# Kernel optimization log

Measured on AMD Instinct MI355X. Metric: run time of the kernel, lower is better.

Reference implementation:

```python
import jax, jax.numpy as jnp
import numpy as np

D_MODEL = 1024
D_FFN = 2048
WINDOW = 64
EPS = 1e-6


def rmsnorm(x, w):
    rms = jnp.sqrt(jnp.mean(x * x, axis=-1, keepdims=True) + EPS)
    return x / rms * w


def setup_inputs() -> dict:
    key = jax.random.key(0)
    ks = jax.random.split(key, 9)
    s = 0.02
    return {
        "x": jax.random.normal(ks[0], (4, 2048, D_MODEL), dtype=jnp.float32),
        "norm1_w": jnp.ones((D_MODEL,), dtype=jnp.float32),
        "norm2_w": jnp.ones((D_MODEL,), dtype=jnp.float32),
        "Wq": jax.random.normal(ks[1], (D_MODEL, D_MODEL), dtype=jnp.float32) * s,
        "Wk": jax.random.normal(ks[2], (D_MODEL, D_MODEL), dtype=jnp.float32) * s,
        "Wv": jax.random.normal(ks[3], (D_MODEL, D_MODEL), dtype=jnp.float32) * s,
        "Wo": jax.random.normal(ks[4], (D_MODEL, D_MODEL), dtype=jnp.float32) * s,
        "W1": jax.random.normal(ks[5], (D_MODEL, D_FFN), dtype=jnp.float32) * s,
        "W2": jax.random.normal(ks[6], (D_FFN, D_MODEL), dtype=jnp.float32) * s,
        "W3": jax.random.normal(ks[7], (D_MODEL, D_FFN), dtype=jnp.float32) * s,
    }


def reference(x, norm1_w, norm2_w, Wq, Wk, Wv, Wo, W1, W2, W3):
    B, T, D = x.shape
    scale = D ** (-0.5)
    residual = x
    xn = rmsnorm(x, norm1_w)
    q = xn @ Wq  # [B,T,D]
    k = xn @ Wk
    v = xn @ Wv
    # causal local-window mask: attend iff 0 <= i-j < WINDOW
    rows = jnp.arange(T)[:, None]
    cols = jnp.arange(T)[None, :]
    mask = (cols <= rows) & (rows - cols < WINDOW)  # [T,T] bool
    scores = jnp.einsum("bid,bjd->bij", q, k) * scale
    scores = jnp.where(mask[None], scores, -jnp.inf)
    weights = jax.nn.softmax(scores, axis=-1)
    attended = jnp.einsum("bij,bjd->bid", weights, v)
    x = residual + attended @ Wo
    # SwiGLU FFN
    xn2 = rmsnorm(x, norm2_w)
    ffn = (jax.nn.silu(xn2 @ W1) * (xn2 @ W3)) @ W2
    return x + ffn
```

## Files before the change

### kernel.cpp

```cpp
#include <hip/hip_runtime.h>
#include <hip/hip_bf16.h>

typedef __attribute__((ext_vector_type(8))) short bf16x8;
typedef __attribute__((ext_vector_type(4))) float f32x4;

__device__ __forceinline__ short to_bf16s(float f) {
    union { __hip_bfloat16 h; short s; } u;
    u.h = __float2bfloat16(f);
    return u.s;
}

__device__ __forceinline__ float bf16s_to_f(short s) {
    union { float f; unsigned u; } cv;
    cv.u = ((unsigned)(unsigned short)s) << 16;
    return cv.f;
}

__device__ __forceinline__ void load_lds16(const void* g, void* l) {
    __builtin_amdgcn_global_load_lds((const __attribute__((address_space(1))) void*)g,
                                     (__attribute__((address_space(3))) void*)l, 16, 0, 0);
}

__global__ __launch_bounds__(256)
void transpose_all(const float* __restrict__ Wq, const float* __restrict__ Wk,
                   const float* __restrict__ Wv, const float* __restrict__ Wo,
                   const float* __restrict__ W1, const float* __restrict__ W3,
                   const float* __restrict__ W2,
                   short* __restrict__ WqT, short* __restrict__ WkT,
                   short* __restrict__ WvT, short* __restrict__ WoT,
                   short* __restrict__ W1T, short* __restrict__ W3T,
                   short* __restrict__ W2T) {
    __shared__ float tile[32][33];
    const int bid = blockIdx.x;
    const float* src; short* dst; int K, N, tl;
    if (bid < 4096) {
        const int wi = bid >> 10; tl = bid & 1023;
        src = wi == 0 ? Wq : wi == 1 ? Wk : wi == 2 ? Wv : Wo;
        dst = wi == 0 ? WqT : wi == 1 ? WkT : wi == 2 ? WvT : WoT;
        K = 1024; N = 1024;
    } else if (bid < 8192) {
        const int wi = (bid - 4096) >> 11; tl = (bid - 4096) & 2047;
        src = wi ? W3 : W1; dst = wi ? W3T : W1T;
        K = 1024; N = 2048;
    } else {
        tl = bid - 8192; src = W2; dst = W2T;
        K = 2048; N = 1024;
    }
    const int nx = N >> 5;
    const int n0 = (tl % nx) * 32, k0 = (tl / nx) * 32;
    const int t = threadIdx.x;
    {
        const int lr = t >> 3, lc = (t & 7) * 4;
        float4 v = *(const float4*)&src[(long)(k0 + lr) * N + n0 + lc];
        tile[lr][lc] = v.x; tile[lr][lc + 1] = v.y;
        tile[lr][lc + 2] = v.z; tile[lr][lc + 3] = v.w;
    }
    __syncthreads();
    {
        const int nr = t >> 3, kc = (t & 7) * 4;
        short4 o;
        o.x = to_bf16s(tile[kc][nr]);
        o.y = to_bf16s(tile[kc + 1][nr]);
        o.z = to_bf16s(tile[kc + 2][nr]);
        o.w = to_bf16s(tile[kc + 3][nr]);
        *(short4*)&dst[(long)(n0 + nr) * K + k0 + kc] = o;
    }
}

__global__ __launch_bounds__(256)
void rmsnorm_kernel(const float* __restrict__ x, const float* __restrict__ wt,
                    short* __restrict__ out) {
    const int D = 1024;
    const long row = blockIdx.x;
    const int t = threadIdx.x;
    float4 v = ((const float4*)(x + row * D))[t];
    float ss = v.x * v.x + v.y * v.y + v.z * v.z + v.w * v.w;
    #pragma unroll
    for (int off = 32; off; off >>= 1) ss += __shfl_xor(ss, off);
    __shared__ float red[4];
    if ((t & 63) == 0) red[t >> 6] = ss;
    __syncthreads();
    ss = red[0] + red[1] + red[2] + red[3];
    const float inv = rsqrtf(ss * (1.0f / 1024.0f) + 1e-6f);
    float4 wv = ((const float4*)wt)[t];
    short4 o;
    o.x = to_bf16s(v.x * inv * wv.x);
    o.y = to_bf16s(v.y * inv * wv.y);
    o.z = to_bf16s(v.z * inv * wv.z);
    o.w = to_bf16s(v.w * inv * wv.w);
    *(short4*)&out[row * D + t * 4] = o;
}

#define MFMA16(MB, NB, BREG)                                                   \
    __builtin_amdgcn_s_barrier();                                              \
    asm volatile("s_waitcnt lgkmcnt(0)" ::: "memory");                         \
    __builtin_amdgcn_sched_barrier(0);                                         \
    __builtin_amdgcn_s_setprio(1);                                             \
    _Pragma("unroll")                                                          \
    for (int m_ = 0; m_ < 4; ++m_)                                             \
        _Pragma("unroll")                                                      \
        for (int n_ = 0; n_ < 2; ++n_) {                                       \
            acc[(MB) + m_][(NB) + n_] = __builtin_amdgcn_mfma_f32_16x16x32_bf16( \
                a[m_][0], BREG[n_][0], acc[(MB) + m_][(NB) + n_], 0, 0, 0);    \
            acc[(MB) + m_][(NB) + n_] = __builtin_amdgcn_mfma_f32_16x16x32_bf16( \
                a[m_][1], BREG[n_][1], acc[(MB) + m_][(NB) + n_], 0, 0, 0);    \
        }                                                                      \
    __builtin_amdgcn_s_setprio(0);                                             \
    __builtin_amdgcn_s_barrier();

#define READA(BUF, MG)                                                         \
    _Pragma("unroll")                                                          \
    for (int m_ = 0; m_ < 4; ++m_) {                                           \
        const int rih_ = ((MG) * 4 + m_) * 16 + lm;                            \
        const int rb_ = ((BUF) * 2 + wr) * 16384 + rih_ * 128;                 \
        a[m_][0] = *(const bf16x8*)&lds[rb_ + ((lk * 16) ^ sw)];               \
        a[m_][1] = *(const bf16x8*)&lds[rb_ + ((64 + lk * 16) ^ sw)];          \
    }

#define READB(BUF, NH, ARR)                                                    \
    _Pragma("unroll")                                                          \
    for (int n_ = 0; n_ < 2; ++n_) {                                           \
        const int rih_ = (wc & 1) * 64 + ((NH) * 2 + n_) * 16 + lm;            \
        const int rb_ = 65536 + ((BUF) * 2 + (wc >> 1)) * 16384 + rih_ * 128;  \
        ARR[n_][0] = *(const bf16x8*)&lds[rb_ + ((lk * 16) ^ sw)];             \
        ARR[n_][1] = *(const bf16x8*)&lds[rb_ + ((64 + lk * 16) ^ sw)];        \
    }

template<int EPI>
__global__ __launch_bounds__(512, 2)
void gemm256(const short* __restrict__ A, const short* __restrict__ B0,
             const short* __restrict__ aux, const float* __restrict__ res,
             void* __restrict__ outp, short* __restrict__ outp2,
             int M, int N, int K) {
    __shared__ __align__(16) char lds[131072];

    const int t = threadIdx.x;
    const int lane = t & 63, w = t >> 6;
    const int wr = w >> 2, wc = w & 3;
    const int lm = lane & 15, lk = lane >> 4;
    const int sw = (lm & 7) << 4;

    const int nbn = N >> 8;
    const int nwg = gridDim.x;
    const int chunk = nwg >> 3;
    const int logical = (blockIdx.x & 7) * chunk + (blockIdx.x >> 3);
    const int bm = logical / nbn, bn = logical - (logical / nbn) * nbn;

    const long Kb = (long)K * 2;
    const char* Ab = (const char*)A;
    const char* Bb = (const char*)B0;

    long srcA[2][2], srcB[2][2];
    {
        const int rowp = t >> 3;
        const int cbx = (t & 7) * 16;
        const int swz = ((t >> 3) & 7) << 4;
        #pragma unroll
        for (int h = 0; h < 2; ++h)
            #pragma unroll
            for (int c = 0; c < 2; ++c) {
                srcA[h][c] = (long)(bm * 256 + h * 128 + c * 64 + rowp) * Kb + (cbx ^ swz);
                srcB[h][c] = (long)(bn * 256 + h * 128 + c * 64 + rowp) * Kb + (cbx ^ swz);
            }
    }
    auto stA = [&](int kt, int h) {
        const int buf = kt & 1;
        #pragma unroll
        for (int c = 0; c < 2; ++c)
            load_lds16(Ab + srcA[h][c] + (long)kt * 128,
                       &lds[(buf * 2 + h) * 16384 + c * 8192 + t * 16]);
    };
    auto stB = [&](int kt, int h) {
        const int buf = kt & 1;
        #pragma unroll
        for (int c = 0; c < 2; ++c)
            load_lds16(Bb + srcB[h][c] + (long)kt * 128,
                       &lds[65536 + (buf * 2 + h) * 16384 + c * 8192 + t * 16]);
    };

    f32x4 acc[8][4] = {};
    bf16x8 a[4][2], b0[2][2], b1[2][2];
    const int nt = K >> 6;

    stB(0, 0); stB(0, 1); stA(0, 0); stA(0, 1); stB(1, 0); stB(1, 1);
    asm volatile("s_waitcnt vmcnt(4)" ::: "memory");
    __builtin_amdgcn_s_barrier();

    for (int kt0 = 0; kt0 < nt; kt0 += 2) {
        const int kt1 = kt0 + 1;
        const bool pf = (kt0 + 2) < nt;

        READA(0, 0); READB(0, 0, b0);
        stA(kt1, 0);
        MFMA16(0, 0, b0)
        READB(0, 1, b1);
        stA(kt1, 1);
        MFMA16(0, 2, b1)
        READA(0, 1);
        if (pf) stB(kt0 + 2, 0);
        MFMA16(4, 2, b1)
        if (pf) { stB(kt0 + 2, 1); asm volatile("s_waitcnt vmcnt(4)" ::: "memory"); }
        else    { asm volatile("s_waitcnt vmcnt(0)" ::: "memory"); }
        MFMA16(4, 0, b0)
        READA(1, 0); READB(1, 0, b0);
        if (pf) stA(kt0 + 2, 0);
        MFMA16(0, 0, b0)
        READB(1, 1, b1);
        if (pf) stA(kt0 + 2, 1);
        MFMA16(0, 2, b1)
        READA(1, 1);
        if (pf) stB(kt1 + 2, 0);
        MFMA16(4, 2, b1)
        if (pf) { stB(kt1 + 2, 1); asm volatile("s_waitcnt vmcnt(4)" ::: "memory"); }
        else    { asm volatile("s_waitcnt vmcnt(0)" ::: "memory"); }
        MFMA16(4, 0, b0)
    }

    #pragma unroll
    for (int mf = 0; mf < 8; ++mf)
      #pragma unroll
      for (int nf = 0; nf < 4; ++nf)
        #pragma unroll
        for (int r = 0; r < 4; ++r) {
            const int grow = bm * 256 + wr * 128 + mf * 16 + lk * 4 + r;
            const int gcol = bn * 256 + wc * 64 + nf * 16 + lm;
            const float v = acc[mf][nf][r];
            if constexpr (EPI == 0) {
                ((short*)outp)[(long)grow * N + gcol] = to_bf16s(v);
            } else if constexpr (EPI == 2) {
                const long i = (long)grow * N + gcol;
                ((float*)outp)[i] = res[i] + v;
            } else if constexpr (EPI == 4) {
                const long i = (long)grow * N + gcol;
                const float g = bf16s_to_f(aux[i]);
                const float sws = g / (1.f + __expf(-g));
                ((short*)outp)[i] = to_bf16s(sws * v);
            } else {
                if (gcol < 2048)
                    ((short*)outp)[(long)grow * 2048 + gcol] = to_bf16s(v);
                else
                    outp2[(long)(gcol - 2048) * 8192 + grow] = to_bf16s(v);
            }
        }
}

__global__ __launch_bounds__(128)
void attn_kernel(const short* __restrict__ Q, const short* __restrict__ Km,
                 int ldq, const short* __restrict__ VT, short* __restrict__ att) {
    const int T = 2048, D = 1024, Mtot = 8192;
    const int bid = blockIdx.x;
    const int b = bid >> 6;
    const int q0 = (bid & 63) << 5;
    const long qrow0 = (long)b * T + q0;
    const int t = threadIdx.x, lane = t & 63, w = t >> 6;

    __shared__ short Qs[32 * 32];
    __shared__ short Ks[96 * 32];
    __shared__ float S_lds[32][100];
    __shared__ short P_lds[32 * 96];
    __shared__ short VTs[128 * 96];

    f32x4 s[6] = {};
    const int trow = t >> 2, tk8 = (t & 3) * 8;
    for (int kt = 0; kt < 32; ++kt) {
        const int k0 = kt << 5;
        load_lds16(Q + (qrow0 + trow) * ldq + k0 + tk8, &Qs[t * 8]);
        #pragma unroll
        for (int s2 = 0; s2 < 3; ++s2) {
            const int krow = s2 * 32 + trow;
            int j = q0 - 64 + krow; if (j < 0) j = 0;
            load_lds16(Km + ((long)b * T + j) * ldq + k0 + tk8, &Ks[(s2 * 128 + t) * 8]);
        }
        __syncthreads();
        const int ko = (lane >> 4) * 8;
        const bf16x8 aq = *(const bf16x8*)&Qs[(w * 16 + (lane & 15)) * 32 + ko];
        #pragma unroll
        for (int n = 0; n < 6; ++n) {
            const bf16x8 bk = *(const bf16x8*)&Ks[(n * 16 + (lane & 15)) * 32 + ko];
            s[n] = __builtin_amdgcn_mfma_f32_16x16x32_bf16(aq, bk, s[n], 0, 0, 0);
        }
        __syncthreads();
    }
    #pragma unroll
    for (int n = 0; n < 6; ++n)
        #pragma unroll
        for (int r = 0; r < 4; ++r)
            S_lds[w * 16 + ((lane >> 4) << 2) + r][n * 16 + (lane & 15)] = s[n][r] * 0.03125f;
    __syncthreads();

    {
        const int row = t >> 2, c0 = (t & 3) * 24;
        float e[24];
        float mx = -1e30f;
        #pragma unroll
        for (int c = 0; c < 24; ++c) {
            const int kj = c0 + c;
            const bool valid = (kj > row) && (kj <= row + 64) && (q0 - 64 + kj >= 0);
            const float sv = valid ? S_lds[row][kj] : -1e30f;
            e[c] = sv;
            mx = fmaxf(mx, sv);
        }
        mx = fmaxf(mx, __shfl_xor(mx, 1));
        mx = fmaxf(mx, __shfl_xor(mx, 2));
        float sum = 0.f;
        #pragma unroll
        for (int c = 0; c < 24; ++c) {
            const float ev = (e[c] > -1e29f) ? __expf(e[c] - mx) : 0.f;
            e[c] = ev; sum += ev;
        }
        sum += __shfl_xor(sum, 1);
        sum += __shfl_xor(sum, 2);
        const float inv = 1.f / sum;
        #pragma unroll
        for (int c = 0; c < 24; ++c)
            P_lds[row * 96 + c0 + c] = to_bf16s(e[c] * inv);
    }
    __syncthreads();

    bf16x8 pa[3];
    {
        const int ko = (lane >> 4) * 8;
        #pragma unroll
        for (int kc = 0; kc < 3; ++kc)
            pa[kc] = *(const bf16x8*)&P_lds[(w * 16 + (lane & 15)) * 96 + kc * 32 + ko];
    }
    for (int dc = 0; dc < 8; ++dc) {
        #pragma unroll
        for (int s2 = 0; s2 < 12; ++s2) {
            const int idx = s2 * 128 + t;
            const int dr = idx / 12, c = idx - dr * 12;
            int j = q0 - 64 + c * 8; if (j < 0) j = 0;
            load_lds16(VT + (long)(dc * 128 + dr) * Mtot + b * T + j, &VTs[idx * 8]);
        }
        __syncthreads();
        f32x4 o[8] = {};
        const int ko = (lane >> 4) * 8;
        #pragma unroll
        for (int kc = 0; kc < 3; ++kc)
            #pragma unroll
            for (int n = 0; n < 8; ++n) {
                const bf16x8 vb = *(const bf16x8*)&VTs[(n * 16 + (lane & 15)) * 96 + kc * 32 + ko];
                o[n] = __builtin_amdgcn_mfma_f32_16x16x32_bf16(pa[kc], vb, o[n], 0, 0, 0);
            }
        __syncthreads();
        #pragma unroll
        for (int n = 0; n < 8; ++n)
            #pragma unroll
            for (int r = 0; r < 4; ++r) {
                const long grow = qrow0 + w * 16 + ((lane >> 4) << 2) + r;
                const int gcol = dc * 128 + n * 16 + (lane & 15);
                att[grow * D + gcol] = to_bf16s(o[n][r]);
            }
    }
}

extern "C" void kernel_launch(void* const* d_in, const int* in_sizes, int n_in,
                              void* d_out, int out_size, void* d_ws, size_t ws_size,
                              hipStream_t stream) {
    const float* x   = (const float*)d_in[0];
    const float* n1w = (const float*)d_in[1];
    const float* n2w = (const float*)d_in[2];
    const float* Wq  = (const float*)d_in[3];
    const float* Wk  = (const float*)d_in[4];
    const float* Wv  = (const float*)d_in[5];
    const float* Wo  = (const float*)d_in[6];
    const float* W1  = (const float*)d_in[7];
    const float* W2  = (const float*)d_in[8];
    const float* W3  = (const float*)d_in[9];

    const int M = 8192;
    char* ws = (char*)d_ws;
    size_t off = 0;
    auto alloc = [&](size_t bytes) { void* p = ws + off; off += (bytes + 255) & ~(size_t)255; return p; };

    short* xn1 = (short*)alloc((size_t)M * 1024 * 2);
    short* qk  = (short*)alloc((size_t)M * 2048 * 2);
    short* vT  = (short*)alloc((size_t)M * 1024 * 2);
    float* x2  = (float*)alloc((size_t)M * 1024 * 4);
    short* WqT = (short*)alloc((size_t)1024 * 1024 * 2);
    short* WkT = (short*)alloc((size_t)1024 * 1024 * 2);
    short* WvT = (short*)alloc((size_t)1024 * 1024 * 2);
    short* WoT = (short*)alloc((size_t)1024 * 1024 * 2);
    short* W1T = (short*)alloc((size_t)2048 * 1024 * 2);
    short* W3T = (short*)alloc((size_t)2048 * 1024 * 2);
    short* W2T = (short*)alloc((size_t)1024 * 2048 * 2);
    short* att = xn1;
    short* xn2 = qk;
    short* g1  = qk + (size_t)M * 1024;

    transpose_all<<<10240, 256, 0, stream>>>(Wq, Wk, Wv, Wo, W1, W3, W2,
                                             WqT, WkT, WvT, WoT, W1T, W3T, W2T);

    rmsnorm_kernel<<<M, 256, 0, stream>>>(x, n1w, xn1);
    gemm256<5><<<384, 512, 0, stream>>>(xn1, WqT, nullptr, nullptr, qk, vT, M, 3072, 1024);
    attn_kernel<<<256, 128, 0, stream>>>(qk, qk + 1024, 2048, vT, att);
    gemm256<2><<<128, 512, 0, stream>>>(att, WoT, nullptr, x, x2, nullptr, M, 1024, 1024);
    rmsnorm_kernel<<<M, 256, 0, stream>>>(x2, n2w, xn2);
    gemm256<0><<<256, 512, 0, stream>>>(xn2, W1T, nullptr, nullptr, g1, nullptr, M, 2048, 1024);
    gemm256<4><<<256, 512, 0, stream>>>(xn2, W3T, g1, nullptr, g1, nullptr, M, 2048, 1024);
    gemm256<2><<<128, 512, 0, stream>>>(g1, W2T, nullptr, x2, (float*)d_out, nullptr, M, 1024, 2048);
}
```

Before: 317.3 us.

## Add 256x128 GEMM tile variant for small-N GEMMs to raise CU occupancy

Templates the GEMM on a B-tile half count so that a 256x128 output tile variant exists, with its own warp layout, LDS layout, prefetch schedule and epilogue indexing. The QKV, Wo and W2 GEMMs switch to this variant, which doubles their workgroup counts (128 becomes 256 and 384 becomes 768) so the 256 CUs are better filled. The cost is lower per-tile operand reuse and more global traffic per FLOP. It also removes the memory clobber and sched_barrier around the MFMA waitcnt, which loosens the ordering the compiler must keep there.

```diff
diff --git a/kernel.cpp b/kernel.cpp
--- a/kernel.cpp
+++ b/kernel.cpp
@@ -93,8 +93,7 @@
 
 #define MFMA16(MB, NB, BREG)                                                   \
     __builtin_amdgcn_s_barrier();                                              \
-    asm volatile("s_waitcnt lgkmcnt(0)" ::: "memory");                         \
-    __builtin_amdgcn_sched_barrier(0);                                         \
+    asm volatile("s_waitcnt lgkmcnt(0)");                                      \
     __builtin_amdgcn_s_setprio(1);                                             \
     _Pragma("unroll")                                                          \
     for (int m_ = 0; m_ < 4; ++m_)                                             \
@@ -108,41 +107,56 @@
     __builtin_amdgcn_s_setprio(0);                                             \
     __builtin_amdgcn_s_barrier();
 
-#define READA(BUF, MG)                                                         \
+#define READA2(BUF, MG)                                                        \
     _Pragma("unroll")                                                          \
     for (int m_ = 0; m_ < 4; ++m_) {                                           \
-        const int rih_ = ((MG) * 4 + m_) * 16 + lm;                            \
-        const int rb_ = ((BUF) * 2 + wr) * 16384 + rih_ * 128;                 \
+        const int rb_ = ((BUF) * 2 + wr) * 16384 + (((MG) * 4 + m_) * 16 + lm) * 128; \
         a[m_][0] = *(const bf16x8*)&lds[rb_ + ((lk * 16) ^ sw)];               \
         a[m_][1] = *(const bf16x8*)&lds[rb_ + ((64 + lk * 16) ^ sw)];          \
     }
-
-#define READB(BUF, NH, ARR)                                                    \
+#define READB2(BUF, NH, ARR)                                                   \
     _Pragma("unroll")                                                          \
     for (int n_ = 0; n_ < 2; ++n_) {                                           \
-        const int rih_ = (wc & 1) * 64 + ((NH) * 2 + n_) * 16 + lm;            \
-        const int rb_ = 65536 + ((BUF) * 2 + (wc >> 1)) * 16384 + rih_ * 128;  \
+        const int rb_ = 65536 + ((BUF) * 2 + (wc >> 1)) * 16384 +              \
+                        ((wc & 1) * 64 + ((NH) * 2 + n_) * 16 + lm) * 128;     \
         ARR[n_][0] = *(const bf16x8*)&lds[rb_ + ((lk * 16) ^ sw)];             \
         ARR[n_][1] = *(const bf16x8*)&lds[rb_ + ((64 + lk * 16) ^ sw)];        \
     }
-
-template<int EPI>
+#define READA1(BUF)                                                            \
+    _Pragma("unroll")                                                          \
+    for (int m_ = 0; m_ < 4; ++m_) {                                           \
+        const int rb_ = ((BUF) * 2 + (wr >> 1)) * 16384 +                      \
+                        ((wr & 1) * 64 + m_ * 16 + lm) * 128;                  \
+        a[m_][0] = *(const bf16x8*)&lds[rb_ + ((lk * 16) ^ sw)];               \
+        a[m_][1] = *(const bf16x8*)&lds[rb_ + ((64 + lk * 16) ^ sw)];          \
+    }
+#define READB1(BUF, NG, ARR)                                                   \
+    _Pragma("unroll")                                                          \
+    for (int n_ = 0; n_ < 2; ++n_) {                                           \
+        const int rb_ = 65536 + ((BUF) * 2 + wc) * 8192 +                      \
+                        (((NG) * 2 + n_) * 16 + lm) * 128;                     \
+        ARR[n_][0] = *(const bf16x8*)&lds[rb_ + ((lk * 16) ^ sw)];             \
+        ARR[n_][1] = *(const bf16x8*)&lds[rb_ + ((64 + lk * 16) ^ sw)];        \
+    }
+
+template<int EPI, int BNH>
 __global__ __launch_bounds__(512, 2)
 void gemm256(const short* __restrict__ A, const short* __restrict__ B0,
              const short* __restrict__ aux, const float* __restrict__ res,
              void* __restrict__ outp, short* __restrict__ outp2,
              int M, int N, int K) {
-    __shared__ __align__(16) char lds[131072];
+    constexpr int BN = BNH * 128;
+    __shared__ __align__(16) char lds[65536 + BNH * 32768];
 
     const int t = threadIdx.x;
     const int lane = t & 63, w = t >> 6;
-    const int wr = w >> 2, wc = w & 3;
+    const int wr = (BNH == 2) ? (w >> 2) : (w >> 1);
+    const int wc = (BNH == 2) ? (w & 3) : (w & 1);
     const int lm = lane & 15, lk = lane >> 4;
     const int sw = (lm & 7) << 4;
 
-    const int nbn = N >> 8;
-    const int nwg = gridDim.x;
-    const int chunk = nwg >> 3;
+    const int nbn = N / BN;
+    const int chunk = gridDim.x >> 3;
     const int logical = (blockIdx.x & 7) * chunk + (blockIdx.x >> 3);
     const int bm = logical / nbn, bn = logical - (logical / nbn) * nbn;
 
@@ -150,18 +164,20 @@
     const char* Ab = (const char*)A;
     const char* Bb = (const char*)B0;
 
-    long srcA[2][2], srcB[2][2];
+    long srcA[2][2], srcB[2][BNH];
     {
         const int rowp = t >> 3;
         const int cbx = (t & 7) * 16;
         const int swz = ((t >> 3) & 7) << 4;
         #pragma unroll
-        for (int h = 0; h < 2; ++h)
+        for (int h = 0; h < 2; ++h) {
             #pragma unroll
-            for (int c = 0; c < 2; ++c) {
+            for (int c = 0; c < 2; ++c)
                 srcA[h][c] = (long)(bm * 256 + h * 128 + c * 64 + rowp) * Kb + (cbx ^ swz);
-                srcB[h][c] = (long)(bn * 256 + h * 128 + c * 64 + rowp) * Kb + (cbx ^ swz);
-            }
+            #pragma unroll
+            for (int c = 0; c < BNH; ++c)
+                srcB[h][c] = (long)(bn * BN + h * (BN / 2) + c * 64 + rowp) * Kb + (cbx ^ swz);
+        }
     }
     auto stA = [&](int kt, int h) {
         const int buf = kt & 1;
@@ -173,57 +189,84 @@
     auto stB = [&](int kt, int h) {
         const int buf = kt & 1;
         #pragma unroll
-        for (int c = 0; c < 2; ++c)
+        for (int c = 0; c < BNH; ++c)
             load_lds16(Bb + srcB[h][c] + (long)kt * 128,
-                       &lds[65536 + (buf * 2 + h) * 16384 + c * 8192 + t * 16]);
+                       &lds[65536 + (buf * 2 + h) * (BNH * 8192) + c * 8192 + t * 16]);
     };
 
-    f32x4 acc[8][4] = {};
+    constexpr int MF = (BNH == 2) ? 8 : 4;
+    f32x4 acc[MF][4] = {};
     bf16x8 a[4][2], b0[2][2], b1[2][2];
     const int nt = K >> 6;
 
-    stB(0, 0); stB(0, 1); stA(0, 0); stA(0, 1); stB(1, 0); stB(1, 1);
-    asm volatile("s_waitcnt vmcnt(4)" ::: "memory");
-    __builtin_amdgcn_s_barrier();
-
-    for (int kt0 = 0; kt0 < nt; kt0 += 2) {
-        const int kt1 = kt0 + 1;
-        const bool pf = (kt0 + 2) < nt;
-
-        READA(0, 0); READB(0, 0, b0);
-        stA(kt1, 0);
-        MFMA16(0, 0, b0)
-        READB(0, 1, b1);
-        stA(kt1, 1);
-        MFMA16(0, 2, b1)
-        READA(0, 1);
-        if (pf) stB(kt0 + 2, 0);
-        MFMA16(4, 2, b1)
-        if (pf) { stB(kt0 + 2, 1); asm volatile("s_waitcnt vmcnt(4)" ::: "memory"); }
-        else    { asm volatile("s_waitcnt vmcnt(0)" ::: "memory"); }
-        MFMA16(4, 0, b0)
-        READA(1, 0); READB(1, 0, b0);
-        if (pf) stA(kt0 + 2, 0);
-        MFMA16(0, 0, b0)
-        READB(1, 1, b1);
-        if (pf) stA(kt0 + 2, 1);
-        MFMA16(0, 2, b1)
-        READA(1, 1);
-        if (pf) stB(kt1 + 2, 0);
-        MFMA16(4, 2, b1)
-        if (pf) { stB(kt1 + 2, 1); asm volatile("s_waitcnt vmcnt(4)" ::: "memory"); }
-        else    { asm volatile("s_waitcnt vmcnt(0)" ::: "memory"); }
-        MFMA16(4, 0, b0)
-    }
-
+    if constexpr (BNH == 2) {
+        stB(0, 0); stB(0, 1); stA(0, 0); stA(0, 1); stB(1, 0); stB(1, 1);
+        asm volatile("s_waitcnt vmcnt(4)" ::: "memory");
+        __builtin_amdgcn_s_barrier();
+
+        for (int u = 0; u < nt; u += 2) {
+            const bool pf = (u + 2) < nt;
+            READA2(0, 0); READB2(0, 0, b0);
+            stA(u + 1, 0);
+            MFMA16(0, 0, b0)
+            READB2(0, 1, b1);
+            stA(u + 1, 1);
+            MFMA16(0, 2, b1)
+            READA2(0, 1);
+            if (pf) stB(u + 2, 0);
+            MFMA16(4, 2, b1)
+            if (pf) { stB(u + 2, 1); asm volatile("s_waitcnt vmcnt(4)" ::: "memory"); }
+            else    { asm volatile("s_waitcnt vmcnt(0)" ::: "memory"); }
+            MFMA16(4, 0, b0)
+            READA2(1, 0); READB2(1, 0, b0);
+            if (pf) stA(u + 2, 0);
+            MFMA16(0, 0, b0)
+            READB2(1, 1, b1);
+            if (pf) stA(u + 2, 1);
+            MFMA16(0, 2, b1)
+            READA2(1, 1);
+            if (pf) stB(u + 3, 0);
+            MFMA16(4, 2, b1)
+            if (pf) { stB(u + 3, 1); asm volatile("s_waitcnt vmcnt(4)" ::: "memory"); }
+            else    { asm volatile("s_waitcnt vmcnt(0)" ::: "memory"); }
+            MFMA16(4, 0, b0)
+        }
+    } else {
+        stA(0, 0); stA(0, 1); stB(0, 0); stB(0, 1);
+        stA(1, 0); stA(1, 1); stB(1, 0); stB(1, 1);
+        asm volatile("s_waitcnt vmcnt(6)" ::: "memory");
+        __builtin_amdgcn_s_barrier();
+
+        for (int u = 0; u < nt; u += 2) {
+            const bool pf = (u + 2) < nt;
+            READA1(0); READB1(0, 0, b0);
+            if (pf) stA(u + 2, 0);
+            MFMA16(0, 0, b0)
+            READB1(0, 1, b1);
+            if (pf) { stA(u + 2, 1); stB(u + 2, 0); stB(u + 2, 1);
+                      asm volatile("s_waitcnt vmcnt(6)" ::: "memory"); }
+            else    { asm volatile("s_waitcnt vmcnt(0)" ::: "memory"); }
+            MFMA16(0, 2, b1)
+            READA1(1); READB1(1, 0, b0);
+            if (pf) stA(u + 3, 0);
+            MFMA16(0, 0, b0)
+            READB1(1, 1, b1);
+            if (pf) { stA(u + 3, 1); stB(u + 3, 0); stB(u + 3, 1);
+                      asm volatile("s_waitcnt vmcnt(6)" ::: "memory"); }
+            else    { asm volatile("s_waitcnt vmcnt(0)" ::: "memory"); }
+            MFMA16(0, 2, b1)
+        }
+    }
+
+    const int wrows = (BNH == 2) ? 128 : 64;
     #pragma unroll
-    for (int mf = 0; mf < 8; ++mf)
+    for (int mf = 0; mf < MF; ++mf)
       #pragma unroll
       for (int nf = 0; nf < 4; ++nf)
         #pragma unroll
         for (int r = 0; r < 4; ++r) {
-            const int grow = bm * 256 + wr * 128 + mf * 16 + lk * 4 + r;
-            const int gcol = bn * 256 + wc * 64 + nf * 16 + lm;
+            const int grow = bm * 256 + wr * wrows + mf * 16 + lk * 4 + r;
+            const int gcol = bn * BN + wc * 64 + nf * 16 + lm;
             const float v = acc[mf][nf][r];
             if constexpr (EPI == 0) {
                 ((short*)outp)[(long)grow * N + gcol] = to_bf16s(v);
@@ -392,11 +435,11 @@
                                              WqT, WkT, WvT, WoT, W1T, W3T, W2T);
 
     rmsnorm_kernel<<<M, 256, 0, stream>>>(x, n1w, xn1);
-    gemm256<5><<<384, 512, 0, stream>>>(xn1, WqT, nullptr, nullptr, qk, vT, M, 3072, 1024);
+    gemm256<5, 1><<<768, 512, 0, stream>>>(xn1, WqT, nullptr, nullptr, qk, vT, M, 3072, 1024);
     attn_kernel<<<256, 128, 0, stream>>>(qk, qk + 1024, 2048, vT, att);
-    gemm256<2><<<128, 512, 0, stream>>>(att, WoT, nullptr, x, x2, nullptr, M, 1024, 1024);
+    gemm256<2, 1><<<256, 512, 0, stream>>>(att, WoT, nullptr, x, x2, nullptr, M, 1024, 1024);
     rmsnorm_kernel<<<M, 256, 0, stream>>>(x2, n2w, xn2);
-    gemm256<0><<<256, 512, 0, stream>>>(xn2, W1T, nullptr, nullptr, g1, nullptr, M, 2048, 1024);
-    gemm256<4><<<256, 512, 0, stream>>>(xn2, W3T, g1, nullptr, g1, nullptr, M, 2048, 1024);
-    gemm256<2><<<128, 512, 0, stream>>>(g1, W2T, nullptr, x2, (float*)d_out, nullptr, M, 1024, 2048);
-}
+    gemm256<0, 2><<<256, 512, 0, stream>>>(xn2, W1T, nullptr, nullptr, g1, nullptr, M, 2048, 1024);
+    gemm256<4, 2><<<256, 512, 0, stream>>>(xn2, W3T, g1, nullptr, g1, nullptr, M, 2048, 1024);
+    gemm256<2, 1><<<256, 512, 0, stream>>>(g1, W2T, nullptr, x2, (float*)d_out, nullptr, M, 1024, 2048);
+}
```

Result: faster. 285.9 us (-9.9%).
